# Kernel tuning notes

Hardware: AMD Instinct MI355X
Metric: run time of the kernel (lower is better)

## Reference

```python
import jax, jax.numpy as jnp
import numpy as np
import math

BS, L, DIM, H = 2, 1024, 1024, 16
DPH = DIM // H            # 64 dim per head
PHI_DIM = DPH * 1         # phi_size_ratio = 1
N_PROJS = 200
MIN_LOG_STD = math.log(1e-5)
SQRT_PHI = math.sqrt(PHI_DIM)


def setup_inputs() -> dict:
    key = jax.random.key(0)
    ks = jax.random.split(key, 8)
    lin = lambda k: jax.random.normal(k, (DIM, DIM), jnp.float32) * 0.02
    return {
        "x": jax.random.normal(ks[0], (BS, L, DIM), jnp.float32),
        "mask": jnp.ones((BS, L), dtype=jnp.bool_),
        "Wq": lin(ks[1]), "bq": jnp.zeros((DIM,), jnp.float32),
        "Wk": lin(ks[2]), "bk": jnp.zeros((DIM,), jnp.float32),
        "Wv": lin(ks[3]), "bv": jnp.zeros((DIM,), jnp.float32),
        "Wo": lin(ks[4]), "bo": jnp.zeros((DIM,), jnp.float32),
        "log_sigma": jnp.zeros((H, 1, DPH), jnp.float32),  # log(1.0) init
        "random_projs": jax.random.normal(ks[5], (N_PROJS, PHI_DIM, DPH), jnp.float32),
    }


def _phi(x, rp_scaled):
    # x: (b, l, h, d); rp_scaled: (h, phi, d). arccos features: relu(proj) / sqrt(phi_dim)
    x = x / jnp.maximum(jnp.linalg.norm(x, axis=-1, keepdims=True), 1e-12)
    px = jnp.einsum('blhd,hpd->blhp', x, rp_scaled)
    return jax.nn.relu(px) / SQRT_PHI


def _causal_rfa(phi_q, phi_k, v):
    # sequential S,z recurrence, time-major scan
    def step(carry, inp):
        S, z = carry
        pk, pq, vt = inp                       # (b,h,phi),(b,h,phi),(b,h,d)
        S = S + pk[..., :, None] * vt[..., None, :]
        z = z + pk
        num = jnp.einsum('bhp,bhpd->bhd', pq, S)
        den = jnp.einsum('bhp,bhp->bh', pq, z)
        return (S, z), num / jnp.maximum(den, 1e-5)[..., None]

    S0 = jnp.zeros((BS, H, PHI_DIM, DPH), jnp.float32)
    z0 = jnp.zeros((BS, H, PHI_DIM), jnp.float32)
    xs = (jnp.transpose(phi_k, (1, 0, 2, 3)),
          jnp.transpose(phi_q, (1, 0, 2, 3)),
          jnp.transpose(v, (1, 0, 2, 3)))
    _, h_t = jax.lax.scan(step, (S0, z0), xs)  # (l, b, h, d)
    return jnp.transpose(h_t, (1, 0, 2, 3))     # (b, l, h, d)


def reference(x, mask, Wq, bq, Wk, bk, Wv, bv, Wo, bo, log_sigma, random_projs):
    q = (x @ Wq.T + bq).reshape(BS, L, H, DPH)
    k = (x @ Wk.T + bk).reshape(BS, L, H, DPH)
    v = (x @ Wv.T + bv).reshape(BS, L, H, DPH)
    # eval mode: proj_id = 0 for every head
    scale = jnp.exp(jnp.maximum(log_sigma, MIN_LOG_STD))                  # (h,1,d)
    rp = scale * jnp.broadcast_to(random_projs[0], (H, PHI_DIM, DPH))     # (h,phi,d)
    phi_q = _phi(q, rp)
    phi_k = _phi(k, rp) * mask[:, :, None, None].astype(jnp.float32)
    h = _causal_rfa(phi_q, phi_k, v)                                      # (b,l,h,d)
    return h.reshape(BS, L, DIM) @ Wo.T + bo
```

## Files before the change

### kernel.cpp

```cpp
#include <hip/hip_runtime.h>


typedef unsigned short ushort_t;
typedef __attribute__((ext_vector_type(8))) __bf16 bf16x8;
typedef __attribute__((ext_vector_type(4))) float f32x4;

#define MLS -11.512925464970229f

__device__ __forceinline__ ushort_t f2b(float f) {
  union { float f; unsigned u; } v; v.f = f;
  unsigned r = v.u + 0x7FFFu + ((v.u >> 16) & 1u);
  return (ushort_t)(r >> 16);
}

__device__ __forceinline__ void gload16(const void* g, void* l) {
  __builtin_amdgcn_global_load_lds((__attribute__((address_space(1))) void*)(void*)g,
                                   (__attribute__((address_space(3))) void*)l, 16, 0, 0);
}

__device__ __forceinline__ f32x4 mfma_bf16(bf16x8 a, bf16x8 b, f32x4 c) {
  return __builtin_amdgcn_mfma_f32_16x16x32_bf16(a, b, c, 0, 0, 0);
}

__global__ __launch_bounds__(256) void convert_kernel(
    const float* __restrict__ x, const float* __restrict__ Wq, const float* __restrict__ Wk,
    const float* __restrict__ Wv, const float* __restrict__ Wo,
    const float* __restrict__ bq, const float* __restrict__ bk, const float* __restrict__ bv,
    const float* __restrict__ lsig, const float* __restrict__ rp0,
    ushort_t* __restrict__ xb, ushort_t* __restrict__ Wcat, ushort_t* __restrict__ Wob,
    float* __restrict__ bcat, float* __restrict__ sclbuf, ushort_t* __restrict__ rpb) {
  const size_t NX = (size_t)1 << 21, NW = (size_t)1 << 20;
  const size_t nch = (NX + 4 * NW) >> 3;
  size_t stride = (size_t)gridDim.x * 256;
  for (size_t i = (size_t)blockIdx.x * 256 + threadIdx.x; i < nch + 1024; i += stride) {
    if (i < nch) {
      size_t e = i << 3;
      const float* src; ushort_t* dst;
      if (e < NX)            { src = x  + e;               dst = xb   + e; }
      else if (e < NX + NW)  { src = Wq + (e - NX);        dst = Wcat + (e - NX); }
      else if (e < NX + 2*NW){ src = Wk + (e - NX - NW);   dst = Wcat + (e - NX); }
      else if (e < NX + 3*NW){ src = Wv + (e - NX - 2*NW); dst = Wcat + (e - NX); }
      else                   { src = Wo + (e - NX - 3*NW); dst = Wob  + (e - NX - 3*NW); }
      float4 a = *(const float4*)src, c = *(const float4*)(src + 4);
      uint4 u;
      u.x = (unsigned)f2b(a.x) | ((unsigned)f2b(a.y) << 16);
      u.y = (unsigned)f2b(a.z) | ((unsigned)f2b(a.w) << 16);
      u.z = (unsigned)f2b(c.x) | ((unsigned)f2b(c.y) << 16);
      u.w = (unsigned)f2b(c.z) | ((unsigned)f2b(c.w) << 16);
      *(uint4*)dst = u;
    } else {
      int j = (int)(i - nch);
      sclbuf[j] = expf(fmaxf(lsig[j], MLS));
      bcat[j] = bq[j]; bcat[1024 + j] = bk[j]; bcat[2048 + j] = bv[j];
#pragma unroll
      for (int jj = 0; jj < 4; ++jj) {
        int pe = j * 4 + jj;
        rpb[pe] = f2b(rp0[pe]);
      }
    }
  }
}

__global__ __launch_bounds__(512, 2) void qkvphi_kernel(
    const ushort_t* __restrict__ A, const ushort_t* __restrict__ Bm,
    const float* __restrict__ bias, const float* __restrict__ sclbuf,
    const ushort_t* __restrict__ rpb,
    ushort_t* __restrict__ phiq, ushort_t* __restrict__ phik, ushort_t* __restrict__ vbT) {
  __shared__ __align__(16) ushort_t smem[40960];
  const int K = 1024;
  int blk = blockIdx.x;
  int hg = blk & 15, by = blk >> 4;
  int m0 = by << 7;
  int tid = threadIdx.x;
  int w = tid >> 6, l = tid & 63;
  int wr = w & 3, wc = w >> 2;
  int lr = l & 15, lg = l >> 4;
  bf16x8 rpf[2][4];
#pragma unroll
  for (int kk = 0; kk < 2; ++kk)
#pragma unroll
    for (int ni = 0; ni < 4; ++ni)
      rpf[kk][ni] = *(const bf16x8*)(rpb + (ni*16 + lr)*64 + kk*32 + lg*8);

  f32x4 acc[2][6] = {};
  auto stage = [&](int buf, int k0) {
    ushort_t* Ad = smem + buf*8192;
    ushort_t* Bd = smem + 16384 + buf*12288;
#pragma unroll
    for (int it = 0; it < 2; ++it) {
      int idx = it*512 + tid, row = idx >> 3, cg = idx & 7;
      gload16(A + (size_t)(m0 + row)*K + k0 + ((cg ^ (row & 7)) << 3), Ad + idx*8);
    }
#pragma unroll
    for (int it = 0; it < 3; ++it) {
      int idx = it*512 + tid, row = idx >> 3, cg = idx & 7;
      int grow = (row >> 6)*1024 + hg*64 + (row & 63);
      gload16(Bm + (size_t)grow*K + k0 + ((cg ^ (row & 7)) << 3), Bd + idx*8);
    }
  };
  auto compute = [&](int buf) {
    const ushort_t* Ab = smem + buf*8192;
    const ushort_t* Bb = smem + 16384 + buf*12288;
#pragma unroll
    for (int kk = 0; kk < 2; ++kk) {
      bf16x8 af[2], bfr[6];
#pragma unroll
      for (int i = 0; i < 2; ++i) {
        int r = wr*32 + i*16 + lr;
        af[i] = *(const bf16x8*)(Ab + r*64 + (((kk*4 + lg) ^ (r & 7)) << 3));
      }
#pragma unroll
      for (int i = 0; i < 6; ++i) {
        int brow = (i < 4) ? (wc*64 + i*16 + lr) : (128 + wc*32 + (i - 4)*16 + lr);
        bfr[i] = *(const bf16x8*)(Bb + brow*64 + (((kk*4 + lg) ^ (brow & 7)) << 3));
      }
#pragma unroll
      for (int mi = 0; mi < 2; ++mi)
#pragma unroll
        for (int ni = 0; ni < 6; ++ni)
          acc[mi][ni] = mfma_bf16(af[mi], bfr[ni], acc[mi][ni]);
    }
  };
  stage(0, 0);
  for (int t = 0; t < 15; ++t) {
    stage((t + 1) & 1, (t + 1) * 64);
    asm volatile("s_waitcnt vmcnt(5)" ::: "memory");
    __builtin_amdgcn_s_barrier();
    compute(t & 1);
    asm volatile("s_waitcnt lgkmcnt(0)" ::: "memory");
    __builtin_amdgcn_s_barrier();
  }
  asm volatile("s_waitcnt vmcnt(0)" ::: "memory");
  __builtin_amdgcn_s_barrier();
  compute(1);
  __syncthreads();

  int b = m0 >> 10, tloc0 = m0 & 1023;
  size_t hbase = ((size_t)(b*16 + hg) << 16);
  {
    ushort_t* Vt = smem + 16384;
    float bv2[2];
#pragma unroll
    for (int j = 0; j < 2; ++j) bv2[j] = bias[2048 + hg*64 + wc*32 + j*16 + lr];
#pragma unroll
    for (int mi = 0; mi < 2; ++mi) {
      int lloc0 = wr*32 + mi*16 + lg*4;
#pragma unroll
      for (int j = 0; j < 2; ++j) {
        int d = wc*32 + j*16 + lr;
        unsigned long long u = 0;
#pragma unroll
        for (int r = 0; r < 4; ++r)
          u |= (unsigned long long)f2b(acc[mi][4 + j][r] + bv2[j]) << (16*r);
        int sv0 = (lloc0 & 7) | ((((lloc0 >> 3) ^ (d & 15)) & 15) << 3);
        *(unsigned long long*)(Vt + d*128 + sv0) = u;
      }
    }
  }
  ushort_t* Ys = smem + w*2048;
  {
    float bias4[4], scl4[4];
#pragma unroll
    for (int ni = 0; ni < 4; ++ni) {
      bias4[ni] = bias[wc*1024 + hg*64 + ni*16 + lr];
      scl4[ni]  = sclbuf[hg*64 + ni*16 + lr];
    }
#pragma unroll
    for (int mi = 0; mi < 2; ++mi) {
      float v4[4][4];
      float ss[4] = {0.f, 0.f, 0.f, 0.f};
#pragma unroll
      for (int ni = 0; ni < 4; ++ni)
#pragma unroll
        for (int r = 0; r < 4; ++r) {
          float vv = acc[mi][ni][r] + bias4[ni];
          v4[ni][r] = vv;
          ss[r] += vv * vv;
        }
#pragma unroll
      for (int r = 0; r < 4; ++r) {
        float s = ss[r];
        s += __shfl_xor(s, 1); s += __shfl_xor(s, 2);
        s += __shfl_xor(s, 4); s += __shfl_xor(s, 8);
        ss[r] = 1.f / fmaxf(sqrtf(s), 1e-12f);
      }
#pragma unroll
      for (int ni = 0; ni < 4; ++ni) {
        int c = ni*16 + lr;
#pragma unroll
        for (int r = 0; r < 4; ++r) {
          int rl = mi*16 + lg*4 + r;
          Ys[rl*64 + (((c >> 3) ^ (rl & 7)) << 3) + (c & 7)] = f2b(v4[ni][r] * ss[r] * scl4[ni]);
        }
      }
    }
  }
  {
    ushort_t* dst = wc ? phik : phiq;
    f32x4 acc2[2][4] = {};
#pragma unroll
    for (int kk = 0; kk < 2; ++kk) {
      bf16x8 af2[2];
#pragma unroll
      for (int mi = 0; mi < 2; ++mi) {
        int rl = mi*16 + lr;
        af2[mi] = *(const bf16x8*)(Ys + rl*64 + (((kk*4 + lg) ^ (rl & 7)) << 3));
      }
#pragma unroll
      for (int mi = 0; mi < 2; ++mi)
#pragma unroll
        for (int ni = 0; ni < 4; ++ni)
          acc2[mi][ni] = mfma_bf16(af2[mi], rpf[kk][ni], acc2[mi][ni]);
    }
    ushort_t* Pt = Ys;
#pragma unroll
    for (int mi = 0; mi < 2; ++mi)
#pragma unroll
      for (int ni = 0; ni < 4; ++ni)
#pragma unroll
        for (int r = 0; r < 4; ++r) {
          int rl = mi*16 + lg*4 + r;
          int p = ni*16 + lr;
          int sp = (p & 7) | ((((p >> 3) ^ (rl & 7)) & 7) << 3);
          Pt[rl*64 + sp] = f2b(fmaxf(acc2[mi][ni][r], 0.f) * 0.125f);
        }
    size_t gp = hbase + (size_t)(tloc0 + wr*32)*64;
#pragma unroll
    for (int i = 0; i < 4; ++i) {
      int chunk = i*64 + l;
      uint4 u = *(const uint4*)(Pt + chunk*8);
      *(uint4*)(dst + gp + chunk*8) = u;
    }
  }
  __syncthreads();
  {
    const ushort_t* Vt = smem + 16384;
    int tile = by & 7;
#pragma unroll
    for (int c = tid; c < 1024; c += 512) {
      int d = c >> 4, off = c & 15;
      uint4 u = *(const uint4*)(Vt + c*8);
      *(uint4*)(vbT + hbase + (size_t)d*1024 + tile*128 + off*8) = u;
    }
  }
}

__global__ __launch_bounds__(256) void outproj_kernel(
    const ushort_t* __restrict__ A, const ushort_t* __restrict__ Bm,
    const float* __restrict__ bias, float* __restrict__ C) {
  __shared__ __align__(16) ushort_t smem[16384];
  const int K = 1024;
  int wid = (blockIdx.x & 7) * 64 + (blockIdx.x >> 3);
  int bx = wid & 15, by = wid >> 4;
  int m0 = by << 6, n0 = bx << 6;
  int tid = threadIdx.x, w = tid >> 6, l = tid & 63;
  int lr = l & 15, lg = l >> 4;
  auto stage = [&](int buf, int k0) {
    ushort_t* Ad = smem + buf*4096;
    ushort_t* Bd = smem + 8192 + buf*4096;
#pragma unroll
    for (int it = 0; it < 2; ++it) {
      int idx = it*256 + tid, row = idx >> 3, cg = idx & 7;
      gload16(A + (size_t)(m0 + row)*K + k0 + ((cg ^ (row & 7)) << 3), Ad + idx*8);
    }
#pragma unroll
    for (int it = 0; it < 2; ++it) {
      int idx = it*256 + tid, row = idx >> 3, cg = idx & 7;
      gload16(Bm + (size_t)(n0 + row)*K + k0 + ((cg ^ (row & 7)) << 3), Bd + idx*8);
    }
  };
  f32x4 acc[4] = {};
  auto compute = [&](int buf) {
    const ushort_t* Ab = smem + buf*4096;
    const ushort_t* Bb = smem + 8192 + buf*4096;
#pragma unroll
    for (int kk = 0; kk < 2; ++kk) {
      int ra = w*16 + lr;
      bf16x8 af = *(const bf16x8*)(Ab + ra*64 + (((kk*4 + lg) ^ (ra & 7)) << 3));
      bf16x8 bfr[4];
#pragma unroll
      for (int i = 0; i < 4; ++i) {
        int rb = i*16 + lr;
        bfr[i] = *(const bf16x8*)(Bb + rb*64 + (((kk*4 + lg) ^ (rb & 7)) << 3));
      }
#pragma unroll
      for (int ni = 0; ni < 4; ++ni)
        acc[ni] = mfma_bf16(af, bfr[ni], acc[ni]);
    }
  };
  stage(0, 0);
  for (int t = 0; t < 15; ++t) {
    stage((t + 1) & 1, (t + 1) * 64);
    asm volatile("s_waitcnt vmcnt(4)" ::: "memory");
    __builtin_amdgcn_s_barrier();
    compute(t & 1);
    asm volatile("s_waitcnt lgkmcnt(0)" ::: "memory");
    __builtin_amdgcn_s_barrier();
  }
  asm volatile("s_waitcnt vmcnt(0)" ::: "memory");
  __builtin_amdgcn_s_barrier();
  compute(1);
#pragma unroll
  for (int ni = 0; ni < 4; ++ni) {
    int col = n0 + ni*16 + lr;
    float bv = bias[col];
#pragma unroll
    for (int r = 0; r < 4; ++r)
      C[(size_t)(m0 + w*16 + lg*4 + r)*1024 + col] = acc[ni][r] + bv;
  }
}

__global__ __launch_bounds__(256) void attn_kernel(
    const ushort_t* __restrict__ phiq, const ushort_t* __restrict__ phik,
    const ushort_t* __restrict__ vbT, ushort_t* __restrict__ hb) {
  __shared__ __align__(16) ushort_t Qs[8192];
  __shared__ __align__(16) ushort_t Kd[2*8192];
  __shared__ __align__(16) ushort_t Vd[2*8192];
  __shared__ __align__(16) ushort_t Ps[16384];
  __shared__ float den_lds[128];
  int blk = blockIdx.x;
  int qt = blk >> 5, bh = blk & 31;
  int b = bh >> 4, h = bh & 15;
  int tid = threadIdx.x, w = tid >> 6, l = tid & 63;
  int lr = l & 15, lg = l >> 4;
  const ushort_t* pq = phiq + ((size_t)bh << 16) + qt*8192;
  const ushort_t* pk = phik + ((size_t)bh << 16);
  const ushort_t* pv = vbT  + ((size_t)bh << 16);
#pragma unroll
  for (int it = 0; it < 4; ++it) {
    int idx = it*256 + tid;
    gload16(pq + idx*8, Qs + idx*8);
  }
  auto stageKV = [&](int buf, int kt) {
#pragma unroll
    for (int it = 0; it < 4; ++it) {
      int idx = it*256 + tid;
      gload16(pk + kt*8192 + idx*8, Kd + buf*8192 + idx*8);
      gload16(pv + (idx >> 4)*1024 + kt*128 + (idx & 15)*8, Vd + buf*8192 + idx*8);
    }
  };
  f32x4 nacc[2][4] = {};
  float den[2] = {0.f, 0.f};
  auto tile = [&](int buf, bool diag) {
    const ushort_t* Ks = Kd + buf*8192;
    const ushort_t* Vs = Vd + buf*8192;
    bf16x8 qf[2][2];
#pragma unroll
    for (int qi = 0; qi < 2; ++qi)
#pragma unroll
      for (int ks = 0; ks < 2; ++ks) {
        int q = w*32 + qi*16 + lr;
        qf[qi][ks] = *(const bf16x8*)(Qs + q*64 + (((ks*4 + lg) ^ (q & 7)) << 3));
      }
    f32x4 sfr[8][2] = {};
#pragma unroll
    for (int kf = 0; kf < 8; ++kf) {
#pragma unroll
      for (int ks = 0; ks < 2; ++ks) {
        int kloc = kf*16 + lr;
        bf16x8 af = *(const bf16x8*)(Ks + kloc*64 + (((ks*4 + lg) ^ (kloc & 7)) << 3));
        sfr[kf][0] = mfma_bf16(af, qf[0][ks], sfr[kf][0]);
        sfr[kf][1] = mfma_bf16(af, qf[1][ks], sfr[kf][1]);
      }
    }
#pragma unroll
    for (int kf = 0; kf < 8; ++kf) {
#pragma unroll
      for (int qi = 0; qi < 2; ++qi) {
        int q = w*32 + qi*16 + lr;
        f32x4 v4 = sfr[kf][qi];
        if (diag) {
          int keyb = kf*16 + lg*4;
#pragma unroll
          for (int r = 0; r < 4; ++r)
            if (keyb + r > q) v4[r] = 0.f;
        }
        den[qi] += v4[0] + v4[1] + v4[2] + v4[3];
        unsigned lo, hi;
        asm("v_cvt_pk_bf16_f32 %0, %1, %2" : "=v"(lo) : "v"(v4[0]), "v"(v4[1]));
        asm("v_cvt_pk_bf16_f32 %0, %1, %2" : "=v"(hi) : "v"(v4[2]), "v"(v4[3]));
        int chunk = (2*kf + (lg >> 1)) ^ (q & 7);
        uint2 u; u.x = lo; u.y = hi;
        *(uint2*)(Ps + q*128 + chunk*8 + (lg & 1)*4) = u;
      }
    }
#pragma unroll
    for (int ks = 0; ks < 4; ++ks) {
      bf16x8 pa[2];
#pragma unroll
      for (int qi = 0; qi < 2; ++qi) {
        int q = w*32 + qi*16 + lr;
        pa[qi] = *(const bf16x8*)(Ps + q*128 + (((4*ks + lg) ^ (q & 7)) << 3));
      }
#pragma unroll
      for (int df = 0; df < 4; ++df) {
        int d = df*16 + lr;
        bf16x8 vf = *(const bf16x8*)(Vs + d*128 + (((4*ks + lg) ^ (d & 15)) << 3));
        nacc[0][df] = mfma_bf16(pa[0], vf, nacc[0][df]);
        nacc[1][df] = mfma_bf16(pa[1], vf, nacc[1][df]);
      }
    }
  };
  stageKV(0, 0);
  for (int kt = 0; kt < qt; ++kt) {
    stageKV((kt + 1) & 1, kt + 1);
    asm volatile("s_waitcnt vmcnt(8)" ::: "memory");
    __builtin_amdgcn_s_barrier();
    tile(kt & 1, false);
    asm volatile("s_waitcnt lgkmcnt(0)" ::: "memory");
    __builtin_amdgcn_s_barrier();
  }
  asm volatile("s_waitcnt vmcnt(0)" ::: "memory");
  __builtin_amdgcn_s_barrier();
  tile(qt & 1, true);
  den[0] += __shfl_xor(den[0], 16); den[0] += __shfl_xor(den[0], 32);
  den[1] += __shfl_xor(den[1], 16); den[1] += __shfl_xor(den[1], 32);
  if (lg == 0) {
    den_lds[w*32 + lr]      = den[0];
    den_lds[w*32 + 16 + lr] = den[1];
  }
  __syncthreads();
#pragma unroll
  for (int qi = 0; qi < 2; ++qi)
#pragma unroll
    for (int df = 0; df < 4; ++df)
#pragma unroll
      for (int r = 0; r < 4; ++r) {
        int qloc = w*32 + qi*16 + lg*4 + r;
        int d = df*16 + lr;
        float dd = fmaxf(den_lds[qloc], 1e-5f);
        float val = nacc[qi][df][r] / dd;
        hb[((size_t)(b*1024 + qt*128 + qloc))*1024 + h*64 + d] = f2b(val);
      }
}

extern "C" void kernel_launch(void* const* d_in, const int* in_sizes, int n_in,
                              void* d_out, int out_size, void* d_ws, size_t ws_size,
                              hipStream_t stream) {
  const float* x  = (const float*)d_in[0];
  const float* Wq = (const float*)d_in[2];
  const float* bq = (const float*)d_in[3];
  const float* Wk = (const float*)d_in[4];
  const float* bk = (const float*)d_in[5];
  const float* Wv = (const float*)d_in[6];
  const float* bv = (const float*)d_in[7];
  const float* Wo = (const float*)d_in[8];
  const float* bo = (const float*)d_in[9];
  const float* ls = (const float*)d_in[10];
  const float* rp = (const float*)d_in[11];

  char* ws = (char*)d_ws;
  size_t off = 0;
  auto alloc = [&](size_t bytes) { char* p = ws + off; off += (bytes + 255) & ~(size_t)255; return p; };
  ushort_t* xb     = (ushort_t*)alloc((size_t)2048*1024*2);
  ushort_t* Wcat   = (ushort_t*)alloc((size_t)3072*1024*2);
  ushort_t* Wob    = (ushort_t*)alloc((size_t)1024*1024*2);
  float*    bcat   = (float*)   alloc((size_t)3072*4);
  float*    sclbuf = (float*)   alloc((size_t)1024*4);
  ushort_t* rpb    = (ushort_t*)alloc((size_t)64*64*2);
  ushort_t* phiq   = (ushort_t*)alloc((size_t)32*1024*64*2);
  ushort_t* phik   = (ushort_t*)alloc((size_t)32*1024*64*2);
  ushort_t* vbT    = (ushort_t*)alloc((size_t)32*64*1024*2);
  ushort_t* hb     = (ushort_t*)alloc((size_t)2048*1024*2);

  convert_kernel<<<1024, 256, 0, stream>>>(x, Wq, Wk, Wv, Wo, bq, bk, bv, ls, rp,
                                           xb, Wcat, Wob, bcat, sclbuf, rpb);
  qkvphi_kernel<<<256, 512, 0, stream>>>(xb, Wcat, bcat, sclbuf, rpb, phiq, phik, vbT);
  attn_kernel<<<256, 256, 0, stream>>>(phiq, phik, vbT, hb);
  outproj_kernel<<<512, 256, 0, stream>>>(hb, Wob, bo, (float*)d_out);
}
```

Before: 60.88 us.

## Halve QKV-phi tile rows, double grid, map heads per XCD, write V directly

The fused QKV projection and phi kernel now uses 64-row M tiles with 256 threads and 512 blocks instead of 128-row tiles with 512 threads. Blocks are remapped so each XCD handles two fixed heads, which keeps their weight slices in that XCD's L2. V is written straight to global memory in the swizzled transposed layout, which drops the LDS staging pass and its extra barrier. The random-projection fragments are now loaded late to reduce register pressure. In exchange, each block reuses the weight tile across fewer rows, so total weight traffic roughly doubles, and the direct V stores are narrow 8-byte writes.

```diff
diff --git a/kernel.cpp b/kernel.cpp
--- a/kernel.cpp
+++ b/kernel.cpp
@@ -61,58 +61,53 @@
   }
 }
 
-__global__ __launch_bounds__(512, 2) void qkvphi_kernel(
+__global__ __launch_bounds__(256, 2) void qkvphi_kernel(
     const ushort_t* __restrict__ A, const ushort_t* __restrict__ Bm,
     const float* __restrict__ bias, const float* __restrict__ sclbuf,
     const ushort_t* __restrict__ rpb,
     ushort_t* __restrict__ phiq, ushort_t* __restrict__ phik, ushort_t* __restrict__ vbT) {
-  __shared__ __align__(16) ushort_t smem[40960];
+  __shared__ __align__(16) ushort_t smem[32768];
   const int K = 1024;
   int blk = blockIdx.x;
-  int hg = blk & 15, by = blk >> 4;
-  int m0 = by << 7;
+  int xcd = blk & 7, i = blk >> 3;
+  int hg = 2*xcd + (i >> 5), by = i & 31;
+  int m0 = by << 6;
   int tid = threadIdx.x;
   int w = tid >> 6, l = tid & 63;
-  int wr = w & 3, wc = w >> 2;
+  int wr = w & 1, wc = w >> 1;
   int lr = l & 15, lg = l >> 4;
-  bf16x8 rpf[2][4];
-#pragma unroll
-  for (int kk = 0; kk < 2; ++kk)
-#pragma unroll
-    for (int ni = 0; ni < 4; ++ni)
-      rpf[kk][ni] = *(const bf16x8*)(rpb + (ni*16 + lr)*64 + kk*32 + lg*8);
 
   f32x4 acc[2][6] = {};
   auto stage = [&](int buf, int k0) {
-    ushort_t* Ad = smem + buf*8192;
-    ushort_t* Bd = smem + 16384 + buf*12288;
+    ushort_t* Ad = smem + buf*4096;
+    ushort_t* Bd = smem + 8192 + buf*12288;
 #pragma unroll
     for (int it = 0; it < 2; ++it) {
-      int idx = it*512 + tid, row = idx >> 3, cg = idx & 7;
+      int idx = it*256 + tid, row = idx >> 3, cg = idx & 7;
       gload16(A + (size_t)(m0 + row)*K + k0 + ((cg ^ (row & 7)) << 3), Ad + idx*8);
     }
 #pragma unroll
-    for (int it = 0; it < 3; ++it) {
-      int idx = it*512 + tid, row = idx >> 3, cg = idx & 7;
+    for (int it = 0; it < 6; ++it) {
+      int idx = it*256 + tid, row = idx >> 3, cg = idx & 7;
       int grow = (row >> 6)*1024 + hg*64 + (row & 63);
       gload16(Bm + (size_t)grow*K + k0 + ((cg ^ (row & 7)) << 3), Bd + idx*8);
     }
   };
   auto compute = [&](int buf) {
-    const ushort_t* Ab = smem + buf*8192;
-    const ushort_t* Bb = smem + 16384 + buf*12288;
+    const ushort_t* Ab = smem + buf*4096;
+    const ushort_t* Bb = smem + 8192 + buf*12288;
 #pragma unroll
     for (int kk = 0; kk < 2; ++kk) {
       bf16x8 af[2], bfr[6];
 #pragma unroll
-      for (int i = 0; i < 2; ++i) {
-        int r = wr*32 + i*16 + lr;
-        af[i] = *(const bf16x8*)(Ab + r*64 + (((kk*4 + lg) ^ (r & 7)) << 3));
-      }
-#pragma unroll
-      for (int i = 0; i < 6; ++i) {
-        int brow = (i < 4) ? (wc*64 + i*16 + lr) : (128 + wc*32 + (i - 4)*16 + lr);
-        bfr[i] = *(const bf16x8*)(Bb + brow*64 + (((kk*4 + lg) ^ (brow & 7)) << 3));
+      for (int ii = 0; ii < 2; ++ii) {
+        int r = wr*32 + ii*16 + lr;
+        af[ii] = *(const bf16x8*)(Ab + r*64 + (((kk*4 + lg) ^ (r & 7)) << 3));
+      }
+#pragma unroll
+      for (int ii = 0; ii < 6; ++ii) {
+        int brow = (ii < 4) ? (wc*64 + ii*16 + lr) : (128 + wc*32 + (ii - 4)*16 + lr);
+        bfr[ii] = *(const bf16x8*)(Bb + brow*64 + (((kk*4 + lg) ^ (brow & 7)) << 3));
       }
 #pragma unroll
       for (int mi = 0; mi < 2; ++mi)
@@ -124,7 +119,7 @@
   stage(0, 0);
   for (int t = 0; t < 15; ++t) {
     stage((t + 1) & 1, (t + 1) * 64);
-    asm volatile("s_waitcnt vmcnt(5)" ::: "memory");
+    asm volatile("s_waitcnt vmcnt(8)" ::: "memory");
     __builtin_amdgcn_s_barrier();
     compute(t & 1);
     asm volatile("s_waitcnt lgkmcnt(0)" ::: "memory");
@@ -138,13 +133,13 @@
   int b = m0 >> 10, tloc0 = m0 & 1023;
   size_t hbase = ((size_t)(b*16 + hg) << 16);
   {
-    ushort_t* Vt = smem + 16384;
     float bv2[2];
 #pragma unroll
     for (int j = 0; j < 2; ++j) bv2[j] = bias[2048 + hg*64 + wc*32 + j*16 + lr];
 #pragma unroll
     for (int mi = 0; mi < 2; ++mi) {
-      int lloc0 = wr*32 + mi*16 + lg*4;
+      int t0 = tloc0 + wr*32 + mi*16 + lg*4;
+      int lloc0 = t0 & 127;
 #pragma unroll
       for (int j = 0; j < 2; ++j) {
         int d = wc*32 + j*16 + lr;
@@ -153,7 +148,7 @@
         for (int r = 0; r < 4; ++r)
           u |= (unsigned long long)f2b(acc[mi][4 + j][r] + bv2[j]) << (16*r);
         int sv0 = (lloc0 & 7) | ((((lloc0 >> 3) ^ (d & 15)) & 15) << 3);
-        *(unsigned long long*)(Vt + d*128 + sv0) = u;
+        *(unsigned long long*)(vbT + hbase + (size_t)d*1024 + (t0 >> 7)*128 + sv0) = u;
       }
     }
   }
@@ -196,6 +191,12 @@
     }
   }
   {
+    bf16x8 rpf[2][4];
+#pragma unroll
+    for (int kk = 0; kk < 2; ++kk)
+#pragma unroll
+      for (int ni = 0; ni < 4; ++ni)
+        rpf[kk][ni] = *(const bf16x8*)(rpb + (ni*16 + lr)*64 + kk*32 + lg*8);
     ushort_t* dst = wc ? phik : phiq;
     f32x4 acc2[2][4] = {};
 #pragma unroll
@@ -226,21 +227,10 @@
         }
     size_t gp = hbase + (size_t)(tloc0 + wr*32)*64;
 #pragma unroll
-    for (int i = 0; i < 4; ++i) {
-      int chunk = i*64 + l;
+    for (int ii = 0; ii < 4; ++ii) {
+      int chunk = ii*64 + l;
       uint4 u = *(const uint4*)(Pt + chunk*8);
       *(uint4*)(dst + gp + chunk*8) = u;
-    }
-  }
-  __syncthreads();
-  {
-    const ushort_t* Vt = smem + 16384;
-    int tile = by & 7;
-#pragma unroll
-    for (int c = tid; c < 1024; c += 512) {
-      int d = c >> 4, off = c & 15;
-      uint4 u = *(const uint4*)(Vt + c*8);
-      *(uint4*)(vbT + hbase + (size_t)d*1024 + tile*128 + off*8) = u;
     }
   }
 }
@@ -465,7 +455,7 @@
 
   convert_kernel<<<1024, 256, 0, stream>>>(x, Wq, Wk, Wv, Wo, bq, bk, bv, ls, rp,
                                            xb, Wcat, Wob, bcat, sclbuf, rpb);
-  qkvphi_kernel<<<256, 512, 0, stream>>>(xb, Wcat, bcat, sclbuf, rpb, phiq, phik, vbT);
+  qkvphi_kernel<<<512, 256, 0, stream>>>(xb, Wcat, bcat, sclbuf, rpb, phiq, phik, vbT);
   attn_kernel<<<256, 256, 0, stream>>>(phiq, phik, vbT, hb);
   outproj_kernel<<<512, 256, 0, stream>>>(hb, Wob, bo, (float*)d_out);
 }
```

Result: no change. 61.43 us (+0.9%).

## Split A/B staging across half-steps and enlarge outproj tile with MFMA priority

Applied to the files above, without the earlier changes.

In the QKV+phi GEMM and the output projection, the per-step load of the next K-slice is split: the A tile is issued before the barrier and the B tile is issued between the two kk halves of compute. This interleaves global-to-LDS traffic with MFMA work, and s_setprio raises wave priority around the MFMA blocks. The output projection also moves from 64x64 to 128x64 tiles (256 blocks instead of 512) for more reuse per block, at the cost of lower occupancy and a larger LDS footprint. The waitcnt values are adjusted so the current buffer is complete before use.

```diff
diff --git a/kernel.cpp b/kernel.cpp
--- a/kernel.cpp
+++ b/kernel.cpp
@@ -83,14 +83,16 @@
       rpf[kk][ni] = *(const bf16x8*)(rpb + (ni*16 + lr)*64 + kk*32 + lg*8);
 
   f32x4 acc[2][6] = {};
-  auto stage = [&](int buf, int k0) {
+  auto stageA = [&](int buf, int k0) {
     ushort_t* Ad = smem + buf*8192;
-    ushort_t* Bd = smem + 16384 + buf*12288;
 #pragma unroll
     for (int it = 0; it < 2; ++it) {
       int idx = it*512 + tid, row = idx >> 3, cg = idx & 7;
       gload16(A + (size_t)(m0 + row)*K + k0 + ((cg ^ (row & 7)) << 3), Ad + idx*8);
     }
+  };
+  auto stageB = [&](int buf, int k0) {
+    ushort_t* Bd = smem + 16384 + buf*12288;
 #pragma unroll
     for (int it = 0; it < 3; ++it) {
       int idx = it*512 + tid, row = idx >> 3, cg = idx & 7;
@@ -98,41 +100,44 @@
       gload16(Bm + (size_t)grow*K + k0 + ((cg ^ (row & 7)) << 3), Bd + idx*8);
     }
   };
-  auto compute = [&](int buf) {
+  auto compute_kk = [&](int buf, int kk) {
     const ushort_t* Ab = smem + buf*8192;
     const ushort_t* Bb = smem + 16384 + buf*12288;
-#pragma unroll
-    for (int kk = 0; kk < 2; ++kk) {
-      bf16x8 af[2], bfr[6];
-#pragma unroll
-      for (int i = 0; i < 2; ++i) {
-        int r = wr*32 + i*16 + lr;
-        af[i] = *(const bf16x8*)(Ab + r*64 + (((kk*4 + lg) ^ (r & 7)) << 3));
-      }
-#pragma unroll
-      for (int i = 0; i < 6; ++i) {
-        int brow = (i < 4) ? (wc*64 + i*16 + lr) : (128 + wc*32 + (i - 4)*16 + lr);
-        bfr[i] = *(const bf16x8*)(Bb + brow*64 + (((kk*4 + lg) ^ (brow & 7)) << 3));
-      }
-#pragma unroll
-      for (int mi = 0; mi < 2; ++mi)
-#pragma unroll
-        for (int ni = 0; ni < 6; ++ni)
-          acc[mi][ni] = mfma_bf16(af[mi], bfr[ni], acc[mi][ni]);
-    }
-  };
-  stage(0, 0);
-  for (int t = 0; t < 15; ++t) {
-    stage((t + 1) & 1, (t + 1) * 64);
-    asm volatile("s_waitcnt vmcnt(5)" ::: "memory");
-    __builtin_amdgcn_s_barrier();
-    compute(t & 1);
+    bf16x8 af[2], bfr[6];
+#pragma unroll
+    for (int ii = 0; ii < 2; ++ii) {
+      int r = wr*32 + ii*16 + lr;
+      af[ii] = *(const bf16x8*)(Ab + r*64 + (((kk*4 + lg) ^ (r & 7)) << 3));
+    }
+#pragma unroll
+    for (int ii = 0; ii < 6; ++ii) {
+      int brow = (ii < 4) ? (wc*64 + ii*16 + lr) : (128 + wc*32 + (ii - 4)*16 + lr);
+      bfr[ii] = *(const bf16x8*)(Bb + brow*64 + (((kk*4 + lg) ^ (brow & 7)) << 3));
+    }
+    __builtin_amdgcn_s_setprio(1);
+#pragma unroll
+    for (int mi = 0; mi < 2; ++mi)
+#pragma unroll
+      for (int ni = 0; ni < 6; ++ni)
+        acc[mi][ni] = mfma_bf16(af[mi], bfr[ni], acc[mi][ni]);
+    __builtin_amdgcn_s_setprio(0);
+  };
+  stageA(0, 0); stageB(0, 0);
+  for (int t = 0; t < 16; ++t) {
+    int cur = t & 1, nxt = cur ^ 1, k1 = (t + 1) * 64;
+    if (t < 15) {
+      stageA(nxt, k1);
+      asm volatile("s_waitcnt vmcnt(2)" ::: "memory");
+    } else {
+      asm volatile("s_waitcnt vmcnt(0)" ::: "memory");
+    }
+    __builtin_amdgcn_s_barrier();
+    compute_kk(cur, 0);
+    if (t < 15) stageB(nxt, k1);
+    compute_kk(cur, 1);
     asm volatile("s_waitcnt lgkmcnt(0)" ::: "memory");
     __builtin_amdgcn_s_barrier();
   }
-  asm volatile("s_waitcnt vmcnt(0)" ::: "memory");
-  __builtin_amdgcn_s_barrier();
-  compute(1);
   __syncthreads();
 
   int b = m0 >> 10, tloc0 = m0 & 1023;
@@ -248,65 +253,79 @@
 __global__ __launch_bounds__(256) void outproj_kernel(
     const ushort_t* __restrict__ A, const ushort_t* __restrict__ Bm,
     const float* __restrict__ bias, float* __restrict__ C) {
-  __shared__ __align__(16) ushort_t smem[16384];
+  __shared__ __align__(16) ushort_t smem[24576];
   const int K = 1024;
-  int wid = (blockIdx.x & 7) * 64 + (blockIdx.x >> 3);
+  int wid = (blockIdx.x & 7) * 32 + (blockIdx.x >> 3);
   int bx = wid & 15, by = wid >> 4;
-  int m0 = by << 6, n0 = bx << 6;
+  int m0 = by << 7, n0 = bx << 6;
   int tid = threadIdx.x, w = tid >> 6, l = tid & 63;
   int lr = l & 15, lg = l >> 4;
-  auto stage = [&](int buf, int k0) {
-    ushort_t* Ad = smem + buf*4096;
-    ushort_t* Bd = smem + 8192 + buf*4096;
-#pragma unroll
-    for (int it = 0; it < 2; ++it) {
+  auto stageA = [&](int buf, int k0) {
+    ushort_t* Ad = smem + buf*8192;
+#pragma unroll
+    for (int it = 0; it < 4; ++it) {
       int idx = it*256 + tid, row = idx >> 3, cg = idx & 7;
       gload16(A + (size_t)(m0 + row)*K + k0 + ((cg ^ (row & 7)) << 3), Ad + idx*8);
     }
+  };
+  auto stageB = [&](int buf, int k0) {
+    ushort_t* Bd = smem + 16384 + buf*4096;
 #pragma unroll
     for (int it = 0; it < 2; ++it) {
       int idx = it*256 + tid, row = idx >> 3, cg = idx & 7;
       gload16(Bm + (size_t)(n0 + row)*K + k0 + ((cg ^ (row & 7)) << 3), Bd + idx*8);
     }
   };
-  f32x4 acc[4] = {};
-  auto compute = [&](int buf) {
-    const ushort_t* Ab = smem + buf*4096;
-    const ushort_t* Bb = smem + 8192 + buf*4096;
-#pragma unroll
-    for (int kk = 0; kk < 2; ++kk) {
-      int ra = w*16 + lr;
-      bf16x8 af = *(const bf16x8*)(Ab + ra*64 + (((kk*4 + lg) ^ (ra & 7)) << 3));
-      bf16x8 bfr[4];
-#pragma unroll
-      for (int i = 0; i < 4; ++i) {
-        int rb = i*16 + lr;
-        bfr[i] = *(const bf16x8*)(Bb + rb*64 + (((kk*4 + lg) ^ (rb & 7)) << 3));
-      }
+  f32x4 acc[2][4] = {};
+  auto compute_kk = [&](int buf, int kk) {
+    const ushort_t* Ab = smem + buf*8192;
+    const ushort_t* Bb = smem + 16384 + buf*4096;
+    bf16x8 af[2], bfr[4];
+#pragma unroll
+    for (int i = 0; i < 2; ++i) {
+      int ra = w*32 + i*16 + lr;
+      af[i] = *(const bf16x8*)(Ab + ra*64 + (((kk*4 + lg) ^ (ra & 7)) << 3));
+    }
+#pragma unroll
+    for (int i = 0; i < 4; ++i) {
+      int rb = i*16 + lr;
+      bfr[i] = *(const bf16x8*)(Bb + rb*64 + (((kk*4 + lg) ^ (rb & 7)) << 3));
+    }
+    __builtin_amdgcn_s_setprio(1);
+#pragma unroll
+    for (int mi = 0; mi < 2; ++mi)
 #pragma unroll
       for (int ni = 0; ni < 4; ++ni)
-        acc[ni] = mfma_bf16(af, bfr[ni], acc[ni]);
-    }
-  };
-  stage(0, 0);
-  for (int t = 0; t < 15; ++t) {
-    stage((t + 1) & 1, (t + 1) * 64);
-    asm volatile("s_waitcnt vmcnt(4)" ::: "memory");
-    __builtin_amdgcn_s_barrier();
-    compute(t & 1);
+        acc[mi][ni] = mfma_bf16(af[mi], bfr[ni], acc[mi][ni]);
+    __builtin_amdgcn_s_setprio(0);
+  };
+  stageA(0, 0); stageB(0, 0);
+  for (int t = 0; t < 16; ++t) {
+    int cur = t & 1, nxt = cur ^ 1, k1 = (t + 1) * 64;
+    if (t < 15) {
+      stageA(nxt, k1);
+      asm volatile("s_waitcnt vmcnt(4)" ::: "memory");
+    } else {
+      asm volatile("s_waitcnt vmcnt(0)" ::: "memory");
+    }
+    __builtin_amdgcn_s_barrier();
+    compute_kk(cur, 0);
+    if (t < 15) stageB(nxt, k1);
+    compute_kk(cur, 1);
     asm volatile("s_waitcnt lgkmcnt(0)" ::: "memory");
     __builtin_amdgcn_s_barrier();
   }
-  asm volatile("s_waitcnt vmcnt(0)" ::: "memory");
-  __builtin_amdgcn_s_barrier();
-  compute(1);
-#pragma unroll
-  for (int ni = 0; ni < 4; ++ni) {
-    int col = n0 + ni*16 + lr;
-    float bv = bias[col];
-#pragma unroll
-    for (int r = 0; r < 4; ++r)
-      C[(size_t)(m0 + w*16 + lg*4 + r)*1024 + col] = acc[ni][r] + bv;
+#pragma unroll
+  for (int mi = 0; mi < 2; ++mi) {
+    int row = m0 + w*32 + mi*16 + lg*4;
+#pragma unroll
+    for (int ni = 0; ni < 4; ++ni) {
+      int col = n0 + ni*16 + lr;
+      float bv = bias[col];
+#pragma unroll
+      for (int r = 0; r < 4; ++r)
+        C[(size_t)(row + r)*1024 + col] = acc[mi][ni][r] + bv;
+    }
   }
 }
 
@@ -467,5 +486,5 @@
                                            xb, Wcat, Wob, bcat, sclbuf, rpb);
   qkvphi_kernel<<<256, 512, 0, stream>>>(xb, Wcat, bcat, sclbuf, rpb, phiq, phik, vbT);
   attn_kernel<<<256, 256, 0, stream>>>(phiq, phik, vbT, hb);
-  outproj_kernel<<<512, 256, 0, stream>>>(hb, Wob, bo, (float*)d_out);
-}
+  outproj_kernel<<<256, 256, 0, stream>>>(hb, Wob, bo, (float*)d_out);
+}
```

Result: slower. 62.46 us (+2.6%).
